# Kernel optimization log

Hardware: AMD Instinct MI355X
Metric: run time of the kernel (lower is better)

Reference implementation:

```python
import jax, jax.numpy as jnp
import numpy as np

ENC_IN = 64
D_MODEL = 512
B, T = 256, 256


def setup_inputs() -> dict:
    key = jax.random.key(0)
    ks = jax.random.split(key, 16)
    d = D_MODEL
    std = 1.0 / np.sqrt(d)
    def w(k, shape):
        return jax.random.normal(k, shape, dtype=jnp.float32) * std
    return {
        'x': jax.random.normal(ks[0], (B, T, ENC_IN), dtype=jnp.float32),
        'Wa': w(ks[1], (d, 2 * d)),
        'Ua': w(ks[2], (d, 2 * d)),
        'ba': jnp.zeros((2 * d,), jnp.float32),
        'Wna': w(ks[3], (d, d)),
        'Una': w(ks[4], (d, d)),
        'bna': jnp.zeros((d,), jnp.float32),
        'WAttn': w(ks[5], (d, d)),
        'UAttn': w(ks[6], (d, d)),
        'VAttn': w(ks[7], (d, d)),
        'Wma': w(ks[8], (d, d)),
        'Uma': w(ks[9], (d, d)),
        'bma': jax.random.normal(ks[10], (d,), dtype=jnp.float32),  # bias init torch.randn, dim==1 so not re-initialized
        'Wm': w(ks[11], (ENC_IN, 2 * d)),
        'Um': w(ks[12], (d, 2 * d)),
        'bm': jnp.zeros((2 * d,), jnp.float32),
        'Whm': w(ks[13], (ENC_IN, d)),
        'Uhm': w(ks[14], (d, d)),
        'bhm': jnp.zeros((d,), jnp.float32),
    }


def reference(x, Wa, Ua, ba, Wna, Una, bna, WAttn, UAttn, VAttn,
              Wma, Uma, bma, Wm, Um, bm, Whm, Uhm, bhm):
    Bsz = x.shape[0]
    H = Wna.shape[0]

    def step(carry, x_t):
        h, N, h_pp = carry           # h = h_{t-1}, h_pp = h_{t-2}
        d_t = h - h_pp               # 0 at t=0, h_0 at t=1, diff otherwise
        gates_A = d_t @ Wa + N @ Ua + ba
        z_A = jax.nn.sigmoid(gates_A[:, :H])
        r_A = jax.nn.sigmoid(gates_A[:, H:])
        hat_N = jnp.tanh(d_t @ Wna + (N * r_A) @ Una + bna)
        N_new = (1.0 - z_A) * N + z_A * hat_N
        score = jnp.tanh(h @ WAttn + N_new @ UAttn) @ VAttn
        alpha = jax.nn.softmax(score, axis=1)
        Omega = alpha * N_new
        m = jnp.tanh(Omega @ Wma + h @ Uma + bma)
        gates_M = x_t @ Wm + m @ Um + bm
        z_M = jax.nn.sigmoid(gates_M[:, :H])
        r_M = jax.nn.sigmoid(gates_M[:, H:])
        hat_h = jnp.tanh(x_t @ Whm + (m * r_M) @ Uhm + bhm)
        h_new = (1.0 - z_M) * h + z_M * hat_h
        return (h_new, N_new, h), h_new

    h0 = jnp.zeros((Bsz, H), x.dtype)
    init = (h0, h0, h0)
    (h_T, N_T, _), hs = jax.lax.scan(step, init, jnp.swapaxes(x, 0, 1))  # hs: [T,B,H]
    hidden_seq = jnp.swapaxes(hs, 0, 1)  # [B,T,H]
    return hidden_seq, (h_T, N_T)
```

## Files before the change

### kernel.cpp

```cpp
#include <hip/hip_runtime.h>

static constexpr int Bsz  = 256;
static constexpr int Tseq = 256;
static constexpr int Hd   = 512;
static constexpr int Ein  = 64;
static constexpr int NBLK = 256;
static constexpr int NTHR = 512;

typedef __attribute__((ext_vector_type(8))) short bf16x8;
typedef __attribute__((ext_vector_type(4))) float f32x4;
typedef unsigned long long u64;

__device__ __forceinline__ float sigm(float x) { return 1.f / (1.f + expf(-x)); }
__device__ __forceinline__ short f2bf(float f) {
  union { float f; unsigned u; } v; v.f = f;
  unsigned r = v.u + 0x7FFFu + ((v.u >> 16) & 1u);
  return (short)(r >> 16);
}
__device__ __forceinline__ float bf2f(short s) {
  union { float f; unsigned u; } v; v.u = ((unsigned)(unsigned short)s) << 16; return v.f;
}

__device__ __forceinline__ void llc_ld4(f32x4& d, const float* p) {
  asm volatile("global_load_dwordx4 %0, %1, off sc0 sc1" : "=v"(d) : "v"(p));
}
__device__ __forceinline__ void llc_ld1(float& d, const float* p) {
  asm volatile("global_load_dword %0, %1, off sc0 sc1" : "=v"(d) : "v"(p));
}
__device__ __forceinline__ void llc_st1(float* p, float v) {
  asm volatile("global_store_dword %0, %1, off sc0 sc1" :: "v"(p), "v"(v) : "memory");
}
__device__ __forceinline__ void vwait() {
  asm volatile("s_waitcnt vmcnt(0)" ::: "memory");
  __builtin_amdgcn_sched_barrier(0);
}

struct KP {
  const float *x, *ba, *bna, *bma, *bm, *bhm;
  const short *Wh[13], *Wl[13];
  float *Hb0, *Hb1, *Hb2, *Nst, *zA, *NrA, *s1, *score, *mbuf, *zM, *mrM, *out;
  unsigned* cnt;
};

__global__ __launch_bounds__(256)
void prepack(const float* __restrict__ W, short* __restrict__ Whi,
             short* __restrict__ Wlo, int N)
{
  __shared__ float lds[32][257];
  const int tid = threadIdx.x;
  const int k0 = blockIdx.y * 32;
  const int n0 = blockIdx.x * 256;
  #pragma unroll
  for (int i = 0; i < 8; ++i) {
    const int flat = (i * 256 + tid) * 4;
    const int r = flat >> 8, c = flat & 255;
    const float4 v = *(const float4*)(W + (size_t)(k0 + r) * N + n0 + c);
    lds[r][c] = v.x; lds[r][c + 1] = v.y; lds[r][c + 2] = v.z; lds[r][c + 3] = v.w;
  }
  __syncthreads();
  const int lane = tid & 63, wv = tid >> 6;
  const int kr = (lane >> 4) * 8;
  const int cc = lane & 15;
  for (int nt = wv; nt < 16; nt += 4) {
    const int ntg = (n0 >> 4) + nt;
    const size_t off = ((size_t)((k0 >> 5) * (N >> 4) + ntg) * 64 + lane) * 8;
    bf16x8 vh, vl;
    #pragma unroll
    for (int j = 0; j < 8; ++j) {
      const float v = lds[kr + j][nt * 16 + cc];
      const short hb = f2bf(v);
      vh[j] = hb; vl[j] = f2bf(v - bf2f(hb));
    }
    *(bf16x8*)(Whi + off) = vh;
    *(bf16x8*)(Wlo + off) = vl;
  }
}

__device__ __forceinline__ const float* task_ptr(const float* src, int ld, int task) {
  const int kc = task >> 6, dl = task & 63;
  return src + (dl & 15) * ld + kc * 32 + ((dl >> 4) << 3);
}
__device__ __forceinline__ void stage_issue(const float* src, int ld, int task,
                                            f32x4& u0, f32x4& u1) {
  const float* p = task_ptr(src, ld, task);
  llc_ld4(u0, p); llc_ld4(u1, p + 4);
}
__device__ __forceinline__ void task_write(int task, f32x4 u0, f32x4 u1,
                                           short* hi, short* lo) {
  const int o = task << 3;
  bf16x8 vh, vl;
  #pragma unroll
  for (int j = 0; j < 4; ++j) {
    const short h0 = f2bf(u0[j]); vh[j]     = h0; vl[j]     = f2bf(u0[j] - bf2f(h0));
    const short h1 = f2bf(u1[j]); vh[j + 4] = h1; vl[j + 4] = f2bf(u1[j] - bf2f(h1));
  }
  *(bf16x8*)(hi + o) = vh;
  *(bf16x8*)(lo + o) = vl;
}

__device__ __forceinline__ void mm(const short* Ah, const short* Al,
                                   const short* __restrict__ Wh,
                                   const short* __restrict__ Wl,
                                   int ntN, int ntg, int kc0, int kc1,
                                   int lane, f32x4& acc)
{
  for (int kc = kc0; kc < kc1; ++kc) {
    const bf16x8 ah = *(const bf16x8*)(Ah + (((kc << 6) | lane) << 3));
    const bf16x8 al = *(const bf16x8*)(Al + (((kc << 6) | lane) << 3));
    const size_t o = ((size_t)((kc * ntN + ntg) << 6 | lane)) << 3;
    const bf16x8 bh = *(const bf16x8*)(Wh + o);
    const bf16x8 bl = *(const bf16x8*)(Wl + o);
    acc = __builtin_amdgcn_mfma_f32_16x16x32_bf16(ah, bh, acc, 0, 0, 0);
    acc = __builtin_amdgcn_mfma_f32_16x16x32_bf16(al, bh, acc, 0, 0, 0);
    acc = __builtin_amdgcn_mfma_f32_16x16x32_bf16(ah, bl, acc, 0, 0, 0);
  }
}

__device__ __forceinline__ void gbar(unsigned* cnt, int stripe, unsigned& ph) {
  asm volatile("s_waitcnt vmcnt(0)" ::: "memory");
  __syncthreads();
  ++ph;
  if (threadIdx.x == 0) {
    __hip_atomic_fetch_add(&cnt[stripe << 4], 1u, __ATOMIC_RELAXED,
                           __HIP_MEMORY_SCOPE_AGENT);
    const unsigned tgt = ph * 16u;
    while (__hip_atomic_load(&cnt[stripe << 4], __ATOMIC_RELAXED,
                             __HIP_MEMORY_SCOPE_AGENT) < tgt)
      __builtin_amdgcn_s_sleep(1);
  }
  __syncthreads();
}

__global__ __launch_bounds__(NTHR, 1)
void dtgru(KP P)
{
  __shared__ short sAh[8192], sAl[8192];
  __shared__ short sBh[8192], sBl[8192];
  __shared__ short sXh[1024], sXl[1024];
  __shared__ float red[1536];
  const int tid = threadIdx.x, lane = tid & 63, wid = tid >> 6;
  const int bid = blockIdx.x;
  const int g = bid & 15;
  const int stripe = bid >> 4;
  const int r0 = stripe << 4;
  unsigned ph = 0;
  float* Hb[3] = {P.Hb0, P.Hb1, P.Hb2};
  float* const Nstr = P.Nst + (r0 << 9);

  #pragma clang loop unroll(disable)
  for (int t = 0; t < Tseq; ++t) {
    float* Hcur = Hb[t % 3];
    float* Hm1  = Hb[(t + 2) % 3];
    float* Hm2  = Hb[(t + 1) % 3];
    const float* Hm1r = Hm1 + (r0 << 9);
    const float* Hm2r = Hm2 + (r0 << 9);

    {
      f32x4 a0,a1,a2,a3, b0,b1,b2,b3, n0,n1,n2,n3;
      stage_issue(Hm1r, 512, tid,       a0, a1);
      stage_issue(Hm2r, 512, tid,       b0, b1);
      stage_issue(Hm1r, 512, tid + 512, a2, a3);
      stage_issue(Hm2r, 512, tid + 512, b2, b3);
      stage_issue(Nstr, 512, tid,       n0, n1);
      stage_issue(Nstr, 512, tid + 512, n2, n3);
      vwait();
      task_write(tid,       a0 - b0, a1 - b1, sAh, sAl);
      task_write(tid + 512, a2 - b2, a3 - b3, sAh, sAl);
      task_write(tid,       n0, n1, sBh, sBl);
      task_write(tid + 512, n2, n3, sBh, sBl);
    }
    __syncthreads();
    {
      f32x4 acc = {0.f, 0.f, 0.f, 0.f};
      const int nt = wid & 3, half = wid >> 2, ntg = (g << 2) | nt;
      if (!half) mm(sAh, sAl, P.Wh[0], P.Wl[0], 64, ntg, 0, 16, lane, acc);
      else       mm(sBh, sBl, P.Wh[1], P.Wl[1], 64, ntg, 0, 16, lane, acc);
      if (half) *(f32x4*)&red[(nt << 8) | (lane << 2)] = acc;
      __syncthreads();
      if (!half) {
        acc += *(f32x4*)&red[(nt << 8) | (lane << 2)];
        const int col = (g << 6) | (nt << 4) | (lane & 15);
        const float b = P.ba[col];
        const int rb = r0 + ((lane >> 4) << 2);
        if (col < 512) {
          #pragma unroll
          for (int i = 0; i < 4; ++i)
            llc_st1(&P.zA[((rb + i) << 9) | col], sigm(acc[i] + b));
        } else {
          const int j = col - 512;
          float nv[4];
          #pragma unroll
          for (int i = 0; i < 4; ++i) llc_ld1(nv[i], &P.Nst[((rb + i) << 9) | j]);
          vwait();
          #pragma unroll
          for (int i = 0; i < 4; ++i)
            llc_st1(&P.NrA[((rb + i) << 9) | j], nv[i] * sigm(acc[i] + b));
        }
      }
    }
    gbar(P.cnt, stripe, ph);

    {
      f32x4 m0,m1,m2,m3;
      stage_issue(P.NrA + (r0 << 9), 512, tid,       m0, m1);
      stage_issue(P.NrA + (r0 << 9), 512, tid + 512, m2, m3);
      vwait();
      task_write(tid,       m0, m1, sBh, sBl);
      task_write(tid + 512, m2, m3, sBh, sBl);
    }
    __syncthreads();
    {
      f32x4 acc = {0.f, 0.f, 0.f, 0.f};
      const int nt = wid & 1, q = wid >> 1, ntg = (g << 1) | nt;
      const int kc0 = (q & 1) << 3;
      if (!(q >> 1)) mm(sAh, sAl, P.Wh[2], P.Wl[2], 32, ntg, kc0, kc0 + 8, lane, acc);
      else           mm(sBh, sBl, P.Wh[3], P.Wl[3], 32, ntg, kc0, kc0 + 8, lane, acc);
      if (q) *(f32x4*)&red[((((q - 1) << 1) | nt) << 8) | (lane << 2)] = acc;
      __syncthreads();
      if (!q) {
        #pragma unroll
        for (int j = 0; j < 3; ++j) acc += *(f32x4*)&red[(((j << 1) | nt) << 8) | (lane << 2)];
        const int col = (g << 5) | (nt << 4) | (lane & 15);
        const float b = P.bna[col];
        const int rb = r0 + ((lane >> 4) << 2);
        float zv[4], nv[4];
        #pragma unroll
        for (int i = 0; i < 4; ++i) {
          const int idx = ((rb + i) << 9) | col;
          llc_ld1(zv[i], &P.zA[idx]); llc_ld1(nv[i], &P.Nst[idx]);
        }
        vwait();
        #pragma unroll
        for (int i = 0; i < 4; ++i) {
          const int idx = ((rb + i) << 9) | col;
          const float hn = tanhf(acc[i] + b);
          llc_st1(&P.Nst[idx], (1.f - zv[i]) * nv[i] + zv[i] * hn);
        }
      }
    }
    gbar(P.cnt, stripe, ph);

    {
      f32x4 a0,a1,a2,a3, n0,n1,n2,n3;
      stage_issue(Hm1r, 512, tid,       a0, a1);
      stage_issue(Hm1r, 512, tid + 512, a2, a3);
      stage_issue(Nstr, 512, tid,       n0, n1);
      stage_issue(Nstr, 512, tid + 512, n2, n3);
      vwait();
      task_write(tid,       a0, a1, sAh, sAl);
      task_write(tid + 512, a2, a3, sAh, sAl);
      task_write(tid,       n0, n1, sBh, sBl);
      task_write(tid + 512, n2, n3, sBh, sBl);
    }
    __syncthreads();
    {
      f32x4 acc = {0.f, 0.f, 0.f, 0.f};
      const int nt = wid & 1, q = wid >> 1, ntg = (g << 1) | nt;
      const int kc0 = (q & 1) << 3;
      if (!(q >> 1)) mm(sAh, sAl, P.Wh[4], P.Wl[4], 32, ntg, kc0, kc0 + 8, lane, acc);
      else           mm(sBh, sBl, P.Wh[5], P.Wl[5], 32, ntg, kc0, kc0 + 8, lane, acc);
      if (q) *(f32x4*)&red[((((q - 1) << 1) | nt) << 8) | (lane << 2)] = acc;
      __syncthreads();
      if (!q) {
        #pragma unroll
        for (int j = 0; j < 3; ++j) acc += *(f32x4*)&red[(((j << 1) | nt) << 8) | (lane << 2)];
        const int col = (g << 5) | (nt << 4) | (lane & 15);
        const int rb = r0 + ((lane >> 4) << 2);
        #pragma unroll
        for (int i = 0; i < 4; ++i)
          llc_st1(&P.s1[((rb + i) << 9) | col], tanhf(acc[i]));
      }
    }
    gbar(P.cnt, stripe, ph);

    {
      f32x4 m0,m1,m2,m3;
      stage_issue(P.s1 + (r0 << 9), 512, tid,       m0, m1);
      stage_issue(P.s1 + (r0 << 9), 512, tid + 512, m2, m3);
      vwait();
      task_write(tid,       m0, m1, sBh, sBl);
      task_write(tid + 512, m2, m3, sBh, sBl);
    }
    __syncthreads();
    {
      f32x4 acc = {0.f, 0.f, 0.f, 0.f};
      const int nt = wid & 1, q = wid >> 1, ntg = (g << 1) | nt;
      mm(sBh, sBl, P.Wh[6], P.Wl[6], 32, ntg, q << 2, (q << 2) + 4, lane, acc);
      if (q) *(f32x4*)&red[((((q - 1) << 1) | nt) << 8) | (lane << 2)] = acc;
      __syncthreads();
      if (!q) {
        #pragma unroll
        for (int j = 0; j < 3; ++j) acc += *(f32x4*)&red[(((j << 1) | nt) << 8) | (lane << 2)];
        const int col = (g << 5) | (nt << 4) | (lane & 15);
        const int rb = r0 + ((lane >> 4) << 2);
        #pragma unroll
        for (int i = 0; i < 4; ++i)
          llc_st1(&P.score[((rb + i) << 9) | col], acc[i]);
      }
    }
    gbar(P.cnt, stripe, ph);

    {
      #pragma unroll
      for (int rr = 0; rr < 2; ++rr) {
        const int row = r0 + (wid << 1) + rr;
        const float* sr = P.score + (row << 9);
        const float* nr = P.Nst + (row << 9);
        const int k0 = lane << 3;
        f32x4 v0, v1, n0, n1;
        llc_ld4(v0, sr + k0); llc_ld4(v1, sr + k0 + 4);
        llc_ld4(n0, nr + k0); llc_ld4(n1, nr + k0 + 4);
        vwait();
        float mx = v0[0];
        #pragma unroll
        for (int j = 1; j < 4; ++j) mx = fmaxf(mx, v0[j]);
        #pragma unroll
        for (int j = 0; j < 4; ++j) mx = fmaxf(mx, v1[j]);
        #pragma unroll
        for (int d = 1; d < 64; d <<= 1) mx = fmaxf(mx, __shfl_xor(mx, d));
        float e[8];
        #pragma unroll
        for (int j = 0; j < 4; ++j) { e[j] = expf(v0[j] - mx); e[j + 4] = expf(v1[j] - mx); }
        float sm = ((e[0] + e[1]) + (e[2] + e[3])) + ((e[4] + e[5]) + (e[6] + e[7]));
        #pragma unroll
        for (int d = 1; d < 64; d <<= 1) sm += __shfl_xor(sm, d);
        const float inv = 1.f / sm;
        float om[8];
        #pragma unroll
        for (int j = 0; j < 4; ++j) { om[j] = e[j] * inv * n0[j]; om[j + 4] = e[j + 4] * inv * n1[j]; }
        short h[8], l[8];
        #pragma unroll
        for (int j = 0; j < 8; ++j) { h[j] = f2bf(om[j]); l[j] = f2bf(om[j] - bf2f(h[j])); }
        const int o = (((lane >> 2) << 6) | (row & 15) | ((lane & 3) << 4)) << 3;
        u64 ph0 = (u64)(unsigned short)h[0] | ((u64)(unsigned short)h[1] << 16)
                | ((u64)(unsigned short)h[2] << 32) | ((u64)(unsigned short)h[3] << 48);
        u64 ph1 = (u64)(unsigned short)h[4] | ((u64)(unsigned short)h[5] << 16)
                | ((u64)(unsigned short)h[6] << 32) | ((u64)(unsigned short)h[7] << 48);
        u64 pl0 = (u64)(unsigned short)l[0] | ((u64)(unsigned short)l[1] << 16)
                | ((u64)(unsigned short)l[2] << 32) | ((u64)(unsigned short)l[3] << 48);
        u64 pl1 = (u64)(unsigned short)l[4] | ((u64)(unsigned short)l[5] << 16)
                | ((u64)(unsigned short)l[6] << 32) | ((u64)(unsigned short)l[7] << 48);
        *(u64*)(sBh + o)     = ph0;
        *(u64*)(sBh + o + 4) = ph1;
        *(u64*)(sBl + o)     = pl0;
        *(u64*)(sBl + o + 4) = pl1;
      }
      __syncthreads();
      f32x4 acc = {0.f, 0.f, 0.f, 0.f};
      const int nt = wid & 1, q = wid >> 1, ntg = (g << 1) | nt;
      const int kc0 = (q & 1) << 3;
      if (!(q >> 1)) mm(sBh, sBl, P.Wh[7], P.Wl[7], 32, ntg, kc0, kc0 + 8, lane, acc);
      else           mm(sAh, sAl, P.Wh[8], P.Wl[8], 32, ntg, kc0, kc0 + 8, lane, acc);
      if (q) *(f32x4*)&red[((((q - 1) << 1) | nt) << 8) | (lane << 2)] = acc;
      __syncthreads();
      if (!q) {
        #pragma unroll
        for (int j = 0; j < 3; ++j) acc += *(f32x4*)&red[(((j << 1) | nt) << 8) | (lane << 2)];
        const int col = (g << 5) | (nt << 4) | (lane & 15);
        const float b = P.bma[col];
        const int rb = r0 + ((lane >> 4) << 2);
        #pragma unroll
        for (int i = 0; i < 4; ++i)
          llc_st1(&P.mbuf[((rb + i) << 9) | col], tanhf(acc[i] + b));
      }
    }
    gbar(P.cnt, stripe, ph);

    {
      f32x4 x0 = {0,0,0,0}, x1 = {0,0,0,0}, m0,m1,m2,m3;
      if (tid < 128)
        stage_issue(P.x + ((size_t)r0 * 256 + t) * 64, Tseq * Ein, tid, x0, x1);
      stage_issue(P.mbuf + (r0 << 9), 512, tid,       m0, m1);
      stage_issue(P.mbuf + (r0 << 9), 512, tid + 512, m2, m3);
      vwait();
      if (tid < 128) task_write(tid, x0, x1, sXh, sXl);
      task_write(tid,       m0, m1, sBh, sBl);
      task_write(tid + 512, m2, m3, sBh, sBl);
    }
    __syncthreads();
    {
      f32x4 acc = {0.f, 0.f, 0.f, 0.f};
      const int nt = wid & 3, half = wid >> 2, ntg = (g << 2) | nt;
      if (!half) {
        mm(sXh, sXl, P.Wh[9],  P.Wl[9],  64, ntg, 0, 2, lane, acc);
        mm(sBh, sBl, P.Wh[10], P.Wl[10], 64, ntg, 0, 7, lane, acc);
      } else {
        mm(sBh, sBl, P.Wh[10], P.Wl[10], 64, ntg, 7, 16, lane, acc);
      }
      if (half) *(f32x4*)&red[(nt << 8) | (lane << 2)] = acc;
      __syncthreads();
      if (!half) {
        acc += *(f32x4*)&red[(nt << 8) | (lane << 2)];
        const int col = (g << 6) | (nt << 4) | (lane & 15);
        const float b = P.bm[col];
        const int rb = r0 + ((lane >> 4) << 2);
        if (col < 512) {
          #pragma unroll
          for (int i = 0; i < 4; ++i)
            llc_st1(&P.zM[((rb + i) << 9) | col], sigm(acc[i] + b));
        } else {
          const int j = col - 512;
          float mv[4];
          #pragma unroll
          for (int i = 0; i < 4; ++i) llc_ld1(mv[i], &P.mbuf[((rb + i) << 9) | j]);
          vwait();
          #pragma unroll
          for (int i = 0; i < 4; ++i)
            llc_st1(&P.mrM[((rb + i) << 9) | j], mv[i] * sigm(acc[i] + b));
        }
      }
    }
    gbar(P.cnt, stripe, ph);

    {
      f32x4 m0,m1,m2,m3;
      stage_issue(P.mrM + (r0 << 9), 512, tid,       m0, m1);
      stage_issue(P.mrM + (r0 << 9), 512, tid + 512, m2, m3);
      vwait();
      task_write(tid,       m0, m1, sBh, sBl);
      task_write(tid + 512, m2, m3, sBh, sBl);
    }
    __syncthreads();
    {
      f32x4 acc = {0.f, 0.f, 0.f, 0.f};
      const int nt = wid & 1, q = wid >> 1, ntg = (g << 1) | nt;
      if (q == 0) {
        mm(sXh, sXl, P.Wh[11], P.Wl[11], 32, ntg, 0, 2, lane, acc);
        mm(sBh, sBl, P.Wh[12], P.Wl[12], 32, ntg, 0, 2, lane, acc);
      } else if (q == 1) mm(sBh, sBl, P.Wh[12], P.Wl[12], 32, ntg, 2, 7, lane, acc);
      else if (q == 2)   mm(sBh, sBl, P.Wh[12], P.Wl[12], 32, ntg, 7, 12, lane, acc);
      else               mm(sBh, sBl, P.Wh[12], P.Wl[12], 32, ntg, 12, 16, lane, acc);
      if (q) *(f32x4*)&red[((((q - 1) << 1) | nt) << 8) | (lane << 2)] = acc;
      __syncthreads();
      if (!q) {
        #pragma unroll
        for (int j = 0; j < 3; ++j) acc += *(f32x4*)&red[(((j << 1) | nt) << 8) | (lane << 2)];
        const int col = (g << 5) | (nt << 4) | (lane & 15);
        const float b = P.bhm[col];
        const int rb = r0 + ((lane >> 4) << 2);
        float zv[4], hv[4];
        #pragma unroll
        for (int i = 0; i < 4; ++i) {
          const int idx = ((rb + i) << 9) | col;
          llc_ld1(zv[i], &P.zM[idx]); llc_ld1(hv[i], &Hm1[idx]);
        }
        vwait();
        #pragma unroll
        for (int i = 0; i < 4; ++i) {
          const int row = rb + i;
          const int idx = (row << 9) | col;
          const float hh = tanhf(acc[i] + b);
          const float hnew = (1.f - zv[i]) * hv[i] + zv[i] * hh;
          llc_st1(&Hcur[idx], hnew);
          P.out[((((size_t)row << 8) | t) << 9) | col] = hnew;
        }
      }
    }
    gbar(P.cnt, stripe, ph);
  }
}

__global__ __launch_bounds__(256)
void initk(float* h1, float* h2, float* n, unsigned* cnt) {
  const int i = blockIdx.x * 256 + threadIdx.x;
  h1[i] = 0.f; h2[i] = 0.f; n[i] = 0.f;
  if (blockIdx.x == 0) cnt[threadIdx.x] = 0u;
}

__global__ __launch_bounds__(256)
void finalize(const float* __restrict__ hT, const float* __restrict__ nT,
              float* __restrict__ oh, float* __restrict__ on) {
  const int i = blockIdx.x * 256 + threadIdx.x;
  float a, b;
  llc_ld1(a, &hT[i]); llc_ld1(b, &nT[i]);
  vwait();
  oh[i] = a; on[i] = b;
}

extern "C" void kernel_launch(void* const* d_in, const int* in_sizes, int n_in,
                              void* d_out, int out_size, void* d_ws, size_t ws_size,
                              hipStream_t stream)
{
  (void)in_sizes; (void)n_in; (void)out_size; (void)ws_size;

  unsigned* cnt = (unsigned*)d_ws;
  float* w = (float*)d_ws + 256;
  const int S = Bsz * Hd;

  KP P{};
  P.x   = (const float*)d_in[0];
  P.ba  = (const float*)d_in[3];
  P.bna = (const float*)d_in[6];
  P.bma = (const float*)d_in[12];
  P.bm  = (const float*)d_in[15];
  P.bhm = (const float*)d_in[18];
  P.Hb0 = w;          P.Hb1 = w + S;      P.Hb2 = w + 2 * S;
  P.Nst = w + 3 * S;  P.zA  = w + 4 * S;  P.NrA = w + 5 * S;
  P.s1  = w + 6 * S;  P.score = w + 7 * S; P.mbuf = w + 8 * S;
  P.zM  = w + 9 * S;  P.mrM = w + 10 * S;
  P.out = (float*)d_out;
  P.cnt = cnt;
  float* out_hT = P.out + (size_t)Bsz * Tseq * Hd;
  float* out_NT = out_hT + S;

  short* wpk = (short*)(w + 11 * S);
  const int widx[13] = {1, 2, 4, 5, 7, 8, 9, 10, 11, 13, 14, 16, 17};
  const int wK[13]   = {512, 512, 512, 512, 512, 512, 512, 512, 512, 64, 512, 64, 512};
  const int wN[13]   = {1024, 1024, 512, 512, 512, 512, 512, 512, 512, 1024, 1024, 512, 512};
  {
    size_t off = 0;
    for (int i = 0; i < 13; ++i) {
      const size_t sz = (size_t)wK[i] * wN[i];
      P.Wh[i] = wpk + off; off += sz;
      P.Wl[i] = wpk + off; off += sz;
    }
  }
  for (int i = 0; i < 13; ++i) {
    dim3 gg(wN[i] / 256, wK[i] / 32);
    prepack<<<gg, 256, 0, stream>>>((const float*)d_in[widx[i]],
                                    (short*)P.Wh[i], (short*)P.Wl[i], wN[i]);
  }

  initk<<<S / 256, 256, 0, stream>>>(P.Hb1, P.Hb2, P.Nst, cnt);

  dtgru<<<NBLK, NTHR, 0, stream>>>(P);

  finalize<<<S / 256, 256, 0, stream>>>(P.Hb0 , P.Nst,
                                        out_hT, out_NT);
}
```

Measured before the change: 20.73 ms.

## Halve block count and keep recurrent state in registers and LDS

Drops from 256 to 128 persistent blocks, so each block computes 64 columns per GEMM and both z and r gate tiles for the same columns. Per-column state (N, h, zA, zM, m) is then kept in registers instead of global buffers. The previous h slice is kept in LDS, so d_t no longer needs a second global read, and x and N are reused from LDS across stages. This cuts global traffic and the extra gate buffers, and halves the participants per barrier, but gives each block more MFMA work and uses more LDS.

```diff
diff --git a/kernel.cpp b/kernel.cpp
--- a/kernel.cpp
+++ b/kernel.cpp
@@ -4,7 +4,7 @@
 static constexpr int Tseq = 256;
 static constexpr int Hd   = 512;
 static constexpr int Ein  = 64;
-static constexpr int NBLK = 256;
+static constexpr int NBLK = 128;
 static constexpr int NTHR = 512;
 
 typedef __attribute__((ext_vector_type(8))) short bf16x8;
@@ -24,9 +24,6 @@
 __device__ __forceinline__ void llc_ld4(f32x4& d, const float* p) {
   asm volatile("global_load_dwordx4 %0, %1, off sc0 sc1" : "=v"(d) : "v"(p));
 }
-__device__ __forceinline__ void llc_ld1(float& d, const float* p) {
-  asm volatile("global_load_dword %0, %1, off sc0 sc1" : "=v"(d) : "v"(p));
-}
 __device__ __forceinline__ void llc_st1(float* p, float v) {
   asm volatile("global_store_dword %0, %1, off sc0 sc1" :: "v"(p), "v"(v) : "memory");
 }
@@ -38,7 +35,7 @@
 struct KP {
   const float *x, *ba, *bna, *bma, *bm, *bhm;
   const short *Wh[13], *Wl[13];
-  float *Hb0, *Hb1, *Hb2, *Nst, *zA, *NrA, *s1, *score, *mbuf, *zM, *mrM, *out;
+  float *Hbuf, *Nst, *NrA, *s1, *score, *mbuf, *mrM, *out;
   unsigned* cnt;
 };
 
@@ -80,11 +77,6 @@
   const int kc = task >> 6, dl = task & 63;
   return src + (dl & 15) * ld + kc * 32 + ((dl >> 4) << 3);
 }
-__device__ __forceinline__ void stage_issue(const float* src, int ld, int task,
-                                            f32x4& u0, f32x4& u1) {
-  const float* p = task_ptr(src, ld, task);
-  llc_ld4(u0, p); llc_ld4(u1, p + 4);
-}
 __device__ __forceinline__ void task_write(int task, f32x4 u0, f32x4 u1,
                                            short* hi, short* lo) {
   const int o = task << 3;
@@ -96,6 +88,16 @@
   }
   *(bf16x8*)(hi + o) = vh;
   *(bf16x8*)(lo + o) = vl;
+}
+
+__device__ __forceinline__ void stageSlice(const float* src, short* hi, short* lo,
+                                           int tid) {
+  f32x4 a0, a1, b0, b1;
+  { const float* p = task_ptr(src, 512, tid);       llc_ld4(a0, p); llc_ld4(a1, p + 4); }
+  { const float* p = task_ptr(src, 512, tid + 512); llc_ld4(b0, p); llc_ld4(b1, p + 4); }
+  vwait();
+  task_write(tid,       a0, a1, hi, lo);
+  task_write(tid + 512, b0, b1, hi, lo);
 }
 
 __device__ __forceinline__ void mm(const short* Ah, const short* Al,
@@ -123,7 +125,7 @@
   if (threadIdx.x == 0) {
     __hip_atomic_fetch_add(&cnt[stripe << 4], 1u, __ATOMIC_RELAXED,
                            __HIP_MEMORY_SCOPE_AGENT);
-    const unsigned tgt = ph * 16u;
+    const unsigned tgt = ph * 8u;
     while (__hip_atomic_load(&cnt[stripe << 4], __ATOMIC_RELAXED,
                              __HIP_MEMORY_SCOPE_AGENT) < tgt)
       __builtin_amdgcn_s_sleep(1);
@@ -136,181 +138,163 @@
 {
   __shared__ short sAh[8192], sAl[8192];
   __shared__ short sBh[8192], sBl[8192];
+  __shared__ short sCh[8192], sCl[8192];
+  __shared__ short sDh[8192], sDl[8192];
   __shared__ short sXh[1024], sXl[1024];
-  __shared__ float red[1536];
+  __shared__ float red[2048];
   const int tid = threadIdx.x, lane = tid & 63, wid = tid >> 6;
   const int bid = blockIdx.x;
-  const int g = bid & 15;
-  const int stripe = bid >> 4;
+  const int g = bid & 7;
+  const int stripe = bid >> 3;
   const int r0 = stripe << 4;
+  const int src = wid >> 2, nt = wid & 3;
+  const int ntb = (g << 2) | nt;
+  const int col5 = (g << 6) | (nt << 4) | (lane & 15);
+  const int rb = r0 + ((lane >> 4) << 2);
   unsigned ph = 0;
-  float* Hb[3] = {P.Hb0, P.Hb1, P.Hb2};
-  float* const Nstr = P.Nst + (r0 << 9);
+  float Nreg[4] = {0,0,0,0}, hreg[4] = {0,0,0,0};
+  float zAreg[4] = {0,0,0,0}, zMreg[4] = {0,0,0,0}, mreg[4] = {0,0,0,0};
+  const float b_az = P.ba[col5],  b_ar = P.ba[col5 + 512];
+  const float b_na = P.bna[col5], b_ma = P.bma[col5];
+  const float b_mz = P.bm[col5],  b_mr = P.bm[col5 + 512];
+  const float b_hm = P.bhm[col5];
+
+  for (int i = tid; i < 2048; i += NTHR) {
+    ((u64*)sBh)[i] = 0; ((u64*)sBl)[i] = 0;
+    ((u64*)sDh)[i] = 0; ((u64*)sDl)[i] = 0;
+  }
+  __syncthreads();
 
   #pragma clang loop unroll(disable)
   for (int t = 0; t < Tseq; ++t) {
-    float* Hcur = Hb[t % 3];
-    float* Hm1  = Hb[(t + 2) % 3];
-    float* Hm2  = Hb[(t + 1) % 3];
-    const float* Hm1r = Hm1 + (r0 << 9);
-    const float* Hm2r = Hm2 + (r0 << 9);
-
-    {
-      f32x4 a0,a1,a2,a3, b0,b1,b2,b3, n0,n1,n2,n3;
-      stage_issue(Hm1r, 512, tid,       a0, a1);
-      stage_issue(Hm2r, 512, tid,       b0, b1);
-      stage_issue(Hm1r, 512, tid + 512, a2, a3);
-      stage_issue(Hm2r, 512, tid + 512, b2, b3);
-      stage_issue(Nstr, 512, tid,       n0, n1);
-      stage_issue(Nstr, 512, tid + 512, n2, n3);
+    {
+      f32x4 u0, u1, v0, v1, x0 = {0,0,0,0}, x1 = {0,0,0,0};
+      const float* Hr = P.Hbuf + (r0 << 9);
+      { const float* p = task_ptr(Hr, 512, tid);       llc_ld4(u0, p); llc_ld4(u1, p + 4); }
+      { const float* p = task_ptr(Hr, 512, tid + 512); llc_ld4(v0, p); llc_ld4(v1, p + 4); }
+      if (tid < 128) {
+        const int dl = tid & 63, kc = tid >> 6;
+        const float* px = P.x + ((size_t)(r0 + (dl & 15)) * Tseq + t) * Ein
+                        + kc * 32 + ((dl >> 4) << 3);
+        x0 = *(const f32x4*)px; x1 = *(const f32x4*)(px + 4);
+      }
       vwait();
-      task_write(tid,       a0 - b0, a1 - b1, sAh, sAl);
-      task_write(tid + 512, a2 - b2, a3 - b3, sAh, sAl);
-      task_write(tid,       n0, n1, sBh, sBl);
-      task_write(tid + 512, n2, n3, sBh, sBl);
-    }
-    __syncthreads();
-    {
-      f32x4 acc = {0.f, 0.f, 0.f, 0.f};
-      const int nt = wid & 3, half = wid >> 2, ntg = (g << 2) | nt;
-      if (!half) mm(sAh, sAl, P.Wh[0], P.Wl[0], 64, ntg, 0, 16, lane, acc);
-      else       mm(sBh, sBl, P.Wh[1], P.Wl[1], 64, ntg, 0, 16, lane, acc);
-      if (half) *(f32x4*)&red[(nt << 8) | (lane << 2)] = acc;
-      __syncthreads();
-      if (!half) {
+      {
+        const int o = tid << 3;
+        const bf16x8 dh = *(const bf16x8*)(sDh + o), dlo = *(const bf16x8*)(sDl + o);
+        f32x4 d0, d1;
+        #pragma unroll
+        for (int j = 0; j < 4; ++j) {
+          d0[j] = u0[j] - (bf2f(dh[j])     + bf2f(dlo[j]));
+          d1[j] = u1[j] - (bf2f(dh[j + 4]) + bf2f(dlo[j + 4]));
+        }
+        task_write(tid, d0, d1, sAh, sAl);
+        task_write(tid, u0, u1, sDh, sDl);
+      }
+      {
+        const int o = (tid + 512) << 3;
+        const bf16x8 dh = *(const bf16x8*)(sDh + o), dlo = *(const bf16x8*)(sDl + o);
+        f32x4 d0, d1;
+        #pragma unroll
+        for (int j = 0; j < 4; ++j) {
+          d0[j] = v0[j] - (bf2f(dh[j])     + bf2f(dlo[j]));
+          d1[j] = v1[j] - (bf2f(dh[j + 4]) + bf2f(dlo[j + 4]));
+        }
+        task_write(tid + 512, d0, d1, sAh, sAl);
+        task_write(tid + 512, v0, v1, sDh, sDl);
+      }
+      if (tid < 128) task_write(tid, x0, x1, sXh, sXl);
+    }
+    __syncthreads();
+    {
+      f32x4 az = {0,0,0,0}, ar = {0,0,0,0};
+      const int zg = (g << 2) | nt, rg = 32 + zg;
+      if (!src) { mm(sAh, sAl, P.Wh[0], P.Wl[0], 64, zg, 0, 16, lane, az);
+                  mm(sAh, sAl, P.Wh[0], P.Wl[0], 64, rg, 0, 16, lane, ar); }
+      else      { mm(sBh, sBl, P.Wh[1], P.Wl[1], 64, zg, 0, 16, lane, az);
+                  mm(sBh, sBl, P.Wh[1], P.Wl[1], 64, rg, 0, 16, lane, ar); }
+      if (src) { *(f32x4*)&red[(((nt << 1) | 0) << 8) | (lane << 2)] = az;
+                 *(f32x4*)&red[(((nt << 1) | 1) << 8) | (lane << 2)] = ar; }
+      __syncthreads();
+      if (!src) {
+        az += *(f32x4*)&red[(((nt << 1) | 0) << 8) | (lane << 2)];
+        ar += *(f32x4*)&red[(((nt << 1) | 1) << 8) | (lane << 2)];
+        #pragma unroll
+        for (int i = 0; i < 4; ++i) {
+          zAreg[i] = sigm(az[i] + b_az);
+          const float rA = sigm(ar[i] + b_ar);
+          llc_st1(&P.NrA[((rb + i) << 9) | col5], Nreg[i] * rA);
+        }
+      }
+    }
+    gbar(P.cnt, stripe, ph);
+
+    stageSlice(P.NrA + (r0 << 9), sBh, sBl, tid);
+    __syncthreads();
+    {
+      f32x4 acc = {0,0,0,0};
+      if (!src) mm(sAh, sAl, P.Wh[2], P.Wl[2], 32, ntb, 0, 16, lane, acc);
+      else      mm(sBh, sBl, P.Wh[3], P.Wl[3], 32, ntb, 0, 16, lane, acc);
+      if (src) *(f32x4*)&red[(nt << 8) | (lane << 2)] = acc;
+      __syncthreads();
+      if (!src) {
         acc += *(f32x4*)&red[(nt << 8) | (lane << 2)];
-        const int col = (g << 6) | (nt << 4) | (lane & 15);
-        const float b = P.ba[col];
-        const int rb = r0 + ((lane >> 4) << 2);
-        if (col < 512) {
-          #pragma unroll
-          for (int i = 0; i < 4; ++i)
-            llc_st1(&P.zA[((rb + i) << 9) | col], sigm(acc[i] + b));
-        } else {
-          const int j = col - 512;
-          float nv[4];
-          #pragma unroll
-          for (int i = 0; i < 4; ++i) llc_ld1(nv[i], &P.Nst[((rb + i) << 9) | j]);
-          vwait();
-          #pragma unroll
-          for (int i = 0; i < 4; ++i)
-            llc_st1(&P.NrA[((rb + i) << 9) | j], nv[i] * sigm(acc[i] + b));
-        }
-      }
-    }
-    gbar(P.cnt, stripe, ph);
-
-    {
-      f32x4 m0,m1,m2,m3;
-      stage_issue(P.NrA + (r0 << 9), 512, tid,       m0, m1);
-      stage_issue(P.NrA + (r0 << 9), 512, tid + 512, m2, m3);
+        #pragma unroll
+        for (int i = 0; i < 4; ++i) {
+          const float hn = tanhf(acc[i] + b_na);
+          const float Nn = (1.f - zAreg[i]) * Nreg[i] + zAreg[i] * hn;
+          Nreg[i] = Nn;
+          llc_st1(&P.Nst[((rb + i) << 9) | col5], Nn);
+        }
+      }
+    }
+    gbar(P.cnt, stripe, ph);
+
+    stageSlice(P.Nst + (r0 << 9), sBh, sBl, tid);
+    __syncthreads();
+    {
+      f32x4 acc = {0,0,0,0};
+      if (!src) mm(sDh, sDl, P.Wh[4], P.Wl[4], 32, ntb, 0, 16, lane, acc);
+      else      mm(sBh, sBl, P.Wh[5], P.Wl[5], 32, ntb, 0, 16, lane, acc);
+      if (src) *(f32x4*)&red[(nt << 8) | (lane << 2)] = acc;
+      __syncthreads();
+      if (!src) {
+        acc += *(f32x4*)&red[(nt << 8) | (lane << 2)];
+        #pragma unroll
+        for (int i = 0; i < 4; ++i)
+          llc_st1(&P.s1[((rb + i) << 9) | col5], tanhf(acc[i]));
+      }
+    }
+    gbar(P.cnt, stripe, ph);
+
+    stageSlice(P.s1 + (r0 << 9), sCh, sCl, tid);
+    __syncthreads();
+    {
+      f32x4 acc = {0,0,0,0};
+      mm(sCh, sCl, P.Wh[6], P.Wl[6], 32, ntb, src ? 8 : 0, src ? 16 : 8, lane, acc);
+      if (src) *(f32x4*)&red[(nt << 8) | (lane << 2)] = acc;
+      __syncthreads();
+      if (!src) {
+        acc += *(f32x4*)&red[(nt << 8) | (lane << 2)];
+        #pragma unroll
+        for (int i = 0; i < 4; ++i)
+          llc_st1(&P.score[((rb + i) << 9) | col5], acc[i]);
+      }
+    }
+    gbar(P.cnt, stripe, ph);
+
+    {
+      const int lr0 = wid << 1;
+      f32x4 s00, s01, s10, s11;
+      llc_ld4(s00, P.score + ((r0 + lr0) << 9) + (lane << 3));
+      llc_ld4(s01, P.score + ((r0 + lr0) << 9) + (lane << 3) + 4);
+      llc_ld4(s10, P.score + ((r0 + lr0 + 1) << 9) + (lane << 3));
+      llc_ld4(s11, P.score + ((r0 + lr0 + 1) << 9) + (lane << 3) + 4);
       vwait();
-      task_write(tid,       m0, m1, sBh, sBl);
-      task_write(tid + 512, m2, m3, sBh, sBl);
-    }
-    __syncthreads();
-    {
-      f32x4 acc = {0.f, 0.f, 0.f, 0.f};
-      const int nt = wid & 1, q = wid >> 1, ntg = (g << 1) | nt;
-      const int kc0 = (q & 1) << 3;
-      if (!(q >> 1)) mm(sAh, sAl, P.Wh[2], P.Wl[2], 32, ntg, kc0, kc0 + 8, lane, acc);
-      else           mm(sBh, sBl, P.Wh[3], P.Wl[3], 32, ntg, kc0, kc0 + 8, lane, acc);
-      if (q) *(f32x4*)&red[((((q - 1) << 1) | nt) << 8) | (lane << 2)] = acc;
-      __syncthreads();
-      if (!q) {
-        #pragma unroll
-        for (int j = 0; j < 3; ++j) acc += *(f32x4*)&red[(((j << 1) | nt) << 8) | (lane << 2)];
-        const int col = (g << 5) | (nt << 4) | (lane & 15);
-        const float b = P.bna[col];
-        const int rb = r0 + ((lane >> 4) << 2);
-        float zv[4], nv[4];
-        #pragma unroll
-        for (int i = 0; i < 4; ++i) {
-          const int idx = ((rb + i) << 9) | col;
-          llc_ld1(zv[i], &P.zA[idx]); llc_ld1(nv[i], &P.Nst[idx]);
-        }
-        vwait();
-        #pragma unroll
-        for (int i = 0; i < 4; ++i) {
-          const int idx = ((rb + i) << 9) | col;
-          const float hn = tanhf(acc[i] + b);
-          llc_st1(&P.Nst[idx], (1.f - zv[i]) * nv[i] + zv[i] * hn);
-        }
-      }
-    }
-    gbar(P.cnt, stripe, ph);
-
-    {
-      f32x4 a0,a1,a2,a3, n0,n1,n2,n3;
-      stage_issue(Hm1r, 512, tid,       a0, a1);
-      stage_issue(Hm1r, 512, tid + 512, a2, a3);
-      stage_issue(Nstr, 512, tid,       n0, n1);
-      stage_issue(Nstr, 512, tid + 512, n2, n3);
-      vwait();
-      task_write(tid,       a0, a1, sAh, sAl);
-      task_write(tid + 512, a2, a3, sAh, sAl);
-      task_write(tid,       n0, n1, sBh, sBl);
-      task_write(tid + 512, n2, n3, sBh, sBl);
-    }
-    __syncthreads();
-    {
-      f32x4 acc = {0.f, 0.f, 0.f, 0.f};
-      const int nt = wid & 1, q = wid >> 1, ntg = (g << 1) | nt;
-      const int kc0 = (q & 1) << 3;
-      if (!(q >> 1)) mm(sAh, sAl, P.Wh[4], P.Wl[4], 32, ntg, kc0, kc0 + 8, lane, acc);
-      else           mm(sBh, sBl, P.Wh[5], P.Wl[5], 32, ntg, kc0, kc0 + 8, lane, acc);
-      if (q) *(f32x4*)&red[((((q - 1) << 1) | nt) << 8) | (lane << 2)] = acc;
-      __syncthreads();
-      if (!q) {
-        #pragma unroll
-        for (int j = 0; j < 3; ++j) acc += *(f32x4*)&red[(((j << 1) | nt) << 8) | (lane << 2)];
-        const int col = (g << 5) | (nt << 4) | (lane & 15);
-        const int rb = r0 + ((lane >> 4) << 2);
-        #pragma unroll
-        for (int i = 0; i < 4; ++i)
-          llc_st1(&P.s1[((rb + i) << 9) | col], tanhf(acc[i]));
-      }
-    }
-    gbar(P.cnt, stripe, ph);
-
-    {
-      f32x4 m0,m1,m2,m3;
-      stage_issue(P.s1 + (r0 << 9), 512, tid,       m0, m1);
-      stage_issue(P.s1 + (r0 << 9), 512, tid + 512, m2, m3);
-      vwait();
-      task_write(tid,       m0, m1, sBh, sBl);
-      task_write(tid + 512, m2, m3, sBh, sBl);
-    }
-    __syncthreads();
-    {
-      f32x4 acc = {0.f, 0.f, 0.f, 0.f};
-      const int nt = wid & 1, q = wid >> 1, ntg = (g << 1) | nt;
-      mm(sBh, sBl, P.Wh[6], P.Wl[6], 32, ntg, q << 2, (q << 2) + 4, lane, acc);
-      if (q) *(f32x4*)&red[((((q - 1) << 1) | nt) << 8) | (lane << 2)] = acc;
-      __syncthreads();
-      if (!q) {
-        #pragma unroll
-        for (int j = 0; j < 3; ++j) acc += *(f32x4*)&red[(((j << 1) | nt) << 8) | (lane << 2)];
-        const int col = (g << 5) | (nt << 4) | (lane & 15);
-        const int rb = r0 + ((lane >> 4) << 2);
-        #pragma unroll
-        for (int i = 0; i < 4; ++i)
-          llc_st1(&P.score[((rb + i) << 9) | col], acc[i]);
-      }
-    }
-    gbar(P.cnt, stripe, ph);
-
-    {
       #pragma unroll
       for (int rr = 0; rr < 2; ++rr) {
-        const int row = r0 + (wid << 1) + rr;
-        const float* sr = P.score + (row << 9);
-        const float* nr = P.Nst + (row << 9);
-        const int k0 = lane << 3;
-        f32x4 v0, v1, n0, n1;
-        llc_ld4(v0, sr + k0); llc_ld4(v1, sr + k0 + 4);
-        llc_ld4(n0, nr + k0); llc_ld4(n1, nr + k0 + 4);
-        vwait();
+        const int lr = lr0 | rr;
+        const f32x4 v0 = rr ? s10 : s00, v1 = rr ? s11 : s01;
         float mx = v0[0];
         #pragma unroll
         for (int j = 1; j < 4; ++j) mx = fmaxf(mx, v0[j]);
@@ -325,134 +309,86 @@
         #pragma unroll
         for (int d = 1; d < 64; d <<= 1) sm += __shfl_xor(sm, d);
         const float inv = 1.f / sm;
-        float om[8];
-        #pragma unroll
-        for (int j = 0; j < 4; ++j) { om[j] = e[j] * inv * n0[j]; om[j + 4] = e[j + 4] * inv * n1[j]; }
-        short h[8], l[8];
-        #pragma unroll
-        for (int j = 0; j < 8; ++j) { h[j] = f2bf(om[j]); l[j] = f2bf(om[j] - bf2f(h[j])); }
-        const int o = (((lane >> 2) << 6) | (row & 15) | ((lane & 3) << 4)) << 3;
-        u64 ph0 = (u64)(unsigned short)h[0] | ((u64)(unsigned short)h[1] << 16)
-                | ((u64)(unsigned short)h[2] << 32) | ((u64)(unsigned short)h[3] << 48);
-        u64 ph1 = (u64)(unsigned short)h[4] | ((u64)(unsigned short)h[5] << 16)
-                | ((u64)(unsigned short)h[6] << 32) | ((u64)(unsigned short)h[7] << 48);
-        u64 pl0 = (u64)(unsigned short)l[0] | ((u64)(unsigned short)l[1] << 16)
-                | ((u64)(unsigned short)l[2] << 32) | ((u64)(unsigned short)l[3] << 48);
-        u64 pl1 = (u64)(unsigned short)l[4] | ((u64)(unsigned short)l[5] << 16)
-                | ((u64)(unsigned short)l[6] << 32) | ((u64)(unsigned short)l[7] << 48);
-        *(u64*)(sBh + o)     = ph0;
-        *(u64*)(sBh + o + 4) = ph1;
-        *(u64*)(sBl + o)     = pl0;
-        *(u64*)(sBl + o + 4) = pl1;
-      }
-      __syncthreads();
-      f32x4 acc = {0.f, 0.f, 0.f, 0.f};
-      const int nt = wid & 1, q = wid >> 1, ntg = (g << 1) | nt;
-      const int kc0 = (q & 1) << 3;
-      if (!(q >> 1)) mm(sBh, sBl, P.Wh[7], P.Wl[7], 32, ntg, kc0, kc0 + 8, lane, acc);
-      else           mm(sAh, sAl, P.Wh[8], P.Wl[8], 32, ntg, kc0, kc0 + 8, lane, acc);
-      if (q) *(f32x4*)&red[((((q - 1) << 1) | nt) << 8) | (lane << 2)] = acc;
-      __syncthreads();
-      if (!q) {
-        #pragma unroll
-        for (int j = 0; j < 3; ++j) acc += *(f32x4*)&red[(((j << 1) | nt) << 8) | (lane << 2)];
-        const int col = (g << 5) | (nt << 4) | (lane & 15);
-        const float b = P.bma[col];
-        const int rb = r0 + ((lane >> 4) << 2);
-        #pragma unroll
-        for (int i = 0; i < 4; ++i)
-          llc_st1(&P.mbuf[((rb + i) << 9) | col], tanhf(acc[i] + b));
-      }
-    }
-    gbar(P.cnt, stripe, ph);
-
-    {
-      f32x4 x0 = {0,0,0,0}, x1 = {0,0,0,0}, m0,m1,m2,m3;
-      if (tid < 128)
-        stage_issue(P.x + ((size_t)r0 * 256 + t) * 64, Tseq * Ein, tid, x0, x1);
-      stage_issue(P.mbuf + (r0 << 9), 512, tid,       m0, m1);
-      stage_issue(P.mbuf + (r0 << 9), 512, tid + 512, m2, m3);
-      vwait();
-      if (tid < 128) task_write(tid, x0, x1, sXh, sXl);
-      task_write(tid,       m0, m1, sBh, sBl);
-      task_write(tid + 512, m2, m3, sBh, sBl);
-    }
-    __syncthreads();
-    {
-      f32x4 acc = {0.f, 0.f, 0.f, 0.f};
-      const int nt = wid & 3, half = wid >> 2, ntg = (g << 2) | nt;
-      if (!half) {
-        mm(sXh, sXl, P.Wh[9],  P.Wl[9],  64, ntg, 0, 2, lane, acc);
-        mm(sBh, sBl, P.Wh[10], P.Wl[10], 64, ntg, 0, 7, lane, acc);
+        const int o = ((((lane >> 2) << 6) | lr | ((lane & 3) << 4)) << 3);
+        const bf16x8 nh = *(const bf16x8*)(sBh + o), nl = *(const bf16x8*)(sBl + o);
+        bf16x8 vh, vl;
+        #pragma unroll
+        for (int j = 0; j < 8; ++j) {
+          const float om = e[j] * inv * (bf2f(nh[j]) + bf2f(nl[j]));
+          const short hb = f2bf(om);
+          vh[j] = hb; vl[j] = f2bf(om - bf2f(hb));
+        }
+        *(bf16x8*)(sCh + o) = vh;
+        *(bf16x8*)(sCl + o) = vl;
+      }
+    }
+    __syncthreads();
+    {
+      f32x4 acc = {0,0,0,0};
+      if (!src) mm(sCh, sCl, P.Wh[7], P.Wl[7], 32, ntb, 0, 16, lane, acc);
+      else      mm(sDh, sDl, P.Wh[8], P.Wl[8], 32, ntb, 0, 16, lane, acc);
+      if (src) *(f32x4*)&red[(nt << 8) | (lane << 2)] = acc;
+      __syncthreads();
+      if (!src) {
+        acc += *(f32x4*)&red[(nt << 8) | (lane << 2)];
+        #pragma unroll
+        for (int i = 0; i < 4; ++i) {
+          const float m = tanhf(acc[i] + b_ma);
+          mreg[i] = m;
+          llc_st1(&P.mbuf[((rb + i) << 9) | col5], m);
+        }
+      }
+    }
+    gbar(P.cnt, stripe, ph);
+
+    stageSlice(P.mbuf + (r0 << 9), sAh, sAl, tid);
+    __syncthreads();
+    {
+      f32x4 az = {0,0,0,0}, ar = {0,0,0,0};
+      const int zg = (g << 2) | nt, rg = 32 + zg;
+      if (!src) {
+        mm(sXh, sXl, P.Wh[9],  P.Wl[9],  64, zg, 0, 2, lane, az);
+        mm(sXh, sXl, P.Wh[9],  P.Wl[9],  64, rg, 0, 2, lane, ar);
+        mm(sAh, sAl, P.Wh[10], P.Wl[10], 64, zg, 0, 7, lane, az);
+        mm(sAh, sAl, P.Wh[10], P.Wl[10], 64, rg, 0, 7, lane, ar);
       } else {
-        mm(sBh, sBl, P.Wh[10], P.Wl[10], 64, ntg, 7, 16, lane, acc);
-      }
-      if (half) *(f32x4*)&red[(nt << 8) | (lane << 2)] = acc;
-      __syncthreads();
-      if (!half) {
+        mm(sAh, sAl, P.Wh[10], P.Wl[10], 64, zg, 7, 16, lane, az);
+        mm(sAh, sAl, P.Wh[10], P.Wl[10], 64, rg, 7, 16, lane, ar);
+      }
+      if (src) { *(f32x4*)&red[(((nt << 1) | 0) << 8) | (lane << 2)] = az;
+                 *(f32x4*)&red[(((nt << 1) | 1) << 8) | (lane << 2)] = ar; }
+      __syncthreads();
+      if (!src) {
+        az += *(f32x4*)&red[(((nt << 1) | 0) << 8) | (lane << 2)];
+        ar += *(f32x4*)&red[(((nt << 1) | 1) << 8) | (lane << 2)];
+        #pragma unroll
+        for (int i = 0; i < 4; ++i) {
+          zMreg[i] = sigm(az[i] + b_mz);
+          const float rM = sigm(ar[i] + b_mr);
+          llc_st1(&P.mrM[((rb + i) << 9) | col5], mreg[i] * rM);
+        }
+      }
+    }
+    gbar(P.cnt, stripe, ph);
+
+    stageSlice(P.mrM + (r0 << 9), sCh, sCl, tid);
+    __syncthreads();
+    {
+      f32x4 acc = {0,0,0,0};
+      if (!src) { mm(sXh, sXl, P.Wh[11], P.Wl[11], 32, ntb, 0, 2, lane, acc);
+                  mm(sCh, sCl, P.Wh[12], P.Wl[12], 32, ntb, 0, 7, lane, acc); }
+      else      { mm(sCh, sCl, P.Wh[12], P.Wl[12], 32, ntb, 7, 16, lane, acc); }
+      if (src) *(f32x4*)&red[(nt << 8) | (lane << 2)] = acc;
+      __syncthreads();
+      if (!src) {
         acc += *(f32x4*)&red[(nt << 8) | (lane << 2)];
-        const int col = (g << 6) | (nt << 4) | (lane & 15);
-        const float b = P.bm[col];
-        const int rb = r0 + ((lane >> 4) << 2);
-        if (col < 512) {
-          #pragma unroll
-          for (int i = 0; i < 4; ++i)
-            llc_st1(&P.zM[((rb + i) << 9) | col], sigm(acc[i] + b));
-        } else {
-          const int j = col - 512;
-          float mv[4];
-          #pragma unroll
-          for (int i = 0; i < 4; ++i) llc_ld1(mv[i], &P.mbuf[((rb + i) << 9) | j]);
-          vwait();
-          #pragma unroll
-          for (int i = 0; i < 4; ++i)
-            llc_st1(&P.mrM[((rb + i) << 9) | j], mv[i] * sigm(acc[i] + b));
-        }
-      }
-    }
-    gbar(P.cnt, stripe, ph);
-
-    {
-      f32x4 m0,m1,m2,m3;
-      stage_issue(P.mrM + (r0 << 9), 512, tid,       m0, m1);
-      stage_issue(P.mrM + (r0 << 9), 512, tid + 512, m2, m3);
-      vwait();
-      task_write(tid,       m0, m1, sBh, sBl);
-      task_write(tid + 512, m2, m3, sBh, sBl);
-    }
-    __syncthreads();
-    {
-      f32x4 acc = {0.f, 0.f, 0.f, 0.f};
-      const int nt = wid & 1, q = wid >> 1, ntg = (g << 1) | nt;
-      if (q == 0) {
-        mm(sXh, sXl, P.Wh[11], P.Wl[11], 32, ntg, 0, 2, lane, acc);
-        mm(sBh, sBl, P.Wh[12], P.Wl[12], 32, ntg, 0, 2, lane, acc);
-      } else if (q == 1) mm(sBh, sBl, P.Wh[12], P.Wl[12], 32, ntg, 2, 7, lane, acc);
-      else if (q == 2)   mm(sBh, sBl, P.Wh[12], P.Wl[12], 32, ntg, 7, 12, lane, acc);
-      else               mm(sBh, sBl, P.Wh[12], P.Wl[12], 32, ntg, 12, 16, lane, acc);
-      if (q) *(f32x4*)&red[((((q - 1) << 1) | nt) << 8) | (lane << 2)] = acc;
-      __syncthreads();
-      if (!q) {
-        #pragma unroll
-        for (int j = 0; j < 3; ++j) acc += *(f32x4*)&red[(((j << 1) | nt) << 8) | (lane << 2)];
-        const int col = (g << 5) | (nt << 4) | (lane & 15);
-        const float b = P.bhm[col];
-        const int rb = r0 + ((lane >> 4) << 2);
-        float zv[4], hv[4];
         #pragma unroll
         for (int i = 0; i < 4; ++i) {
-          const int idx = ((rb + i) << 9) | col;
-          llc_ld1(zv[i], &P.zM[idx]); llc_ld1(hv[i], &Hm1[idx]);
-        }
-        vwait();
-        #pragma unroll
-        for (int i = 0; i < 4; ++i) {
-          const int row = rb + i;
-          const int idx = (row << 9) | col;
-          const float hh = tanhf(acc[i] + b);
-          const float hnew = (1.f - zv[i]) * hv[i] + zv[i] * hh;
-          llc_st1(&Hcur[idx], hnew);
-          P.out[((((size_t)row << 8) | t) << 9) | col] = hnew;
+          const float hh = tanhf(acc[i] + b_hm);
+          const float hn = (1.f - zMreg[i]) * hreg[i] + zMreg[i] * hh;
+          hreg[i] = hn;
+          llc_st1(&P.Hbuf[((rb + i) << 9) | col5], hn);
+          P.out[((((size_t)(rb + i)) << 8 | t) << 9) | col5] = hn;
         }
       }
     }
@@ -461,9 +397,9 @@
 }
 
 __global__ __launch_bounds__(256)
-void initk(float* h1, float* h2, float* n, unsigned* cnt) {
+void initk(float* hbuf, unsigned* cnt) {
   const int i = blockIdx.x * 256 + threadIdx.x;
-  h1[i] = 0.f; h2[i] = 0.f; n[i] = 0.f;
+  hbuf[i] = 0.f;
   if (blockIdx.x == 0) cnt[threadIdx.x] = 0u;
 }
 
@@ -471,10 +407,11 @@
 void finalize(const float* __restrict__ hT, const float* __restrict__ nT,
               float* __restrict__ oh, float* __restrict__ on) {
   const int i = blockIdx.x * 256 + threadIdx.x;
-  float a, b;
-  llc_ld1(a, &hT[i]); llc_ld1(b, &nT[i]);
+  f32x4 a, b;
+  asm volatile("global_load_dword %0, %1, off sc0 sc1" : "=v"(a[0]) : "v"(&hT[i]));
+  asm volatile("global_load_dword %0, %1, off sc0 sc1" : "=v"(b[0]) : "v"(&nT[i]));
   vwait();
-  oh[i] = a; on[i] = b;
+  oh[i] = a[0]; on[i] = b[0];
 }
 
 extern "C" void kernel_launch(void* const* d_in, const int* in_sizes, int n_in,
@@ -494,16 +431,15 @@
   P.bma = (const float*)d_in[12];
   P.bm  = (const float*)d_in[15];
   P.bhm = (const float*)d_in[18];
-  P.Hb0 = w;          P.Hb1 = w + S;      P.Hb2 = w + 2 * S;
-  P.Nst = w + 3 * S;  P.zA  = w + 4 * S;  P.NrA = w + 5 * S;
-  P.s1  = w + 6 * S;  P.score = w + 7 * S; P.mbuf = w + 8 * S;
-  P.zM  = w + 9 * S;  P.mrM = w + 10 * S;
+  P.Hbuf = w;          P.Nst = w + S;      P.NrA = w + 2 * S;
+  P.s1   = w + 3 * S;  P.score = w + 4 * S;
+  P.mbuf = w + 5 * S;  P.mrM = w + 6 * S;
   P.out = (float*)d_out;
   P.cnt = cnt;
   float* out_hT = P.out + (size_t)Bsz * Tseq * Hd;
   float* out_NT = out_hT + S;
 
-  short* wpk = (short*)(w + 11 * S);
+  short* wpk = (short*)(w + 7 * S);
   const int widx[13] = {1, 2, 4, 5, 7, 8, 9, 10, 11, 13, 14, 16, 17};
   const int wK[13]   = {512, 512, 512, 512, 512, 512, 512, 512, 512, 64, 512, 64, 512};
   const int wN[13]   = {1024, 1024, 512, 512, 512, 512, 512, 512, 512, 1024, 1024, 512, 512};
@@ -521,10 +457,9 @@
                                     (short*)P.Wh[i], (short*)P.Wl[i], wN[i]);
   }
 
-  initk<<<S / 256, 256, 0, stream>>>(P.Hb1, P.Hb2, P.Nst, cnt);
+  initk<<<S / 256, 256, 0, stream>>>(P.Hbuf, cnt);
 
   dtgru<<<NBLK, NTHR, 0, stream>>>(P);
 
-  finalize<<<S / 256, 256, 0, stream>>>(P.Hb0 , P.Nst,
-                                        out_hT, out_NT);
-}
+  finalize<<<S / 256, 256, 0, stream>>>(P.Hbuf, P.Nst, out_hT, out_NT);
+}
```

Result: slower. 30.08 ms (+45.1%).
